# Performance work log

Hardware: AMD Instinct MI355X
Metric: run time of the kernel (lower is better)

## Reference

```python
import jax, jax.numpy as jnp
import numpy as np

L, F = 3, 6                 # levels, temporal abstraction factor
B, T0, E = 64, 36, 1024     # batch, bottom-level timesteps, encoded-obs dim
S, D, H = 128, 1024, 1024   # stoch size, deter (GRU) size, embed size
O = S + D                   # cell 'output' size (posterior sample ++ det_state)
MIN_STD = 1e-4


def _params(key):
    ks = jax.random.split(key, 10)
    w = lambda k, *s: jax.random.normal(k, s, jnp.float32) * 0.02
    z = lambda *s: jnp.zeros(s, jnp.float32)
    return dict(
        w1=w(ks[0], L, S + O, H), b1=z(L, H),
        gru_wi=w(ks[1], L, H, 3 * D), gru_wh=w(ks[2], L, D, 3 * D),
        gru_bi=z(L, 3 * D), gru_bh=z(L, 3 * D),
        w2=w(ks[3], L, D, H), b2=z(L, H),
        wpm=w(ks[4], L, H, S), bpm=z(L, S),
        wps=w(ks[5], L, H, S), bps=z(L, S),
        q1=w(ks[6], L, D + E, H), qb1=z(L, H),
        q2=w(ks[7], L, H, H), qb2=z(L, H),
        wqm=w(ks[8], L, H, S), bqm=z(L, S),
        wqs=w(ks[9], L, H, S), bqs=z(L, S))


def setup_inputs() -> dict:
    key = jax.random.key(0)
    ks = jax.random.split(key, 10)
    inp = {}
    for l in range(L):
        T = T0 // F ** l  # 36, 6, 1
        inp[f"x{l}"] = jax.random.normal(ks[l], (B, T, E), jnp.float32)
        inp[f"np{l}"] = jax.random.normal(ks[3 + l], (B, T, S), jnp.float32)
        inp[f"nq{l}"] = jax.random.normal(ks[6 + l], (B, T, S), jnp.float32)
    inp.update(_params(ks[9]))
    return inp


def _run_level(p, x, context, ep, eq):
    """Scan one RSSM cell over time. x: [B,T,E], context: [B,T,O]."""
    b = x.shape[0]
    init = (jnp.zeros((b, S), x.dtype), jnp.zeros((b, D), x.dtype))

    def step(carry, inp):
        sample, det = carry
        obs, ctx, e_p, e_q = inp
        # --- prior: dense(sample ++ context) -> GRU -> dense -> (mean, std) ---
        h = jax.nn.elu(jnp.concatenate([sample, ctx], -1) @ p["w1"] + p["b1"])
        gi = h @ p["gru_wi"] + p["gru_bi"]
        gh = det @ p["gru_wh"] + p["gru_bh"]
        gi_r, gi_z, gi_n = jnp.split(gi, 3, -1)
        gh_r, gh_z, gh_n = jnp.split(gh, 3, -1)
        r = jax.nn.sigmoid(gi_r + gh_r)
        zt = jax.nn.sigmoid(gi_z + gh_z)
        n = jnp.tanh(gi_n + r * gh_n)
        det_new = (1.0 - zt) * n + zt * det
        h2 = jax.nn.elu(det_new @ p["w2"] + p["b2"])
        p_mean = h2 @ p["wpm"] + p["bpm"]
        p_std = jax.nn.softplus(h2 @ p["wps"] + p["bps"]) + MIN_STD
        p_sample = p_mean + p_std * e_p  # reparameterized prior draw (unused downstream when use_obs)
        # --- posterior: dense(det ++ obs) -> dense -> (mean, std); use_obs=True ---
        hq = jax.nn.elu(jnp.concatenate([det_new, obs], -1) @ p["q1"] + p["qb1"])
        hq = jax.nn.elu(hq @ p["q2"] + p["qb2"])
        q_mean = hq @ p["wqm"] + p["bqm"]
        q_std = jax.nn.softplus(hq @ p["wqs"] + p["bqs"]) + MIN_STD
        q_sample = q_mean + q_std * e_q
        out = jnp.concatenate([q_sample, det_new], -1)  # posterior['output']
        return (q_sample, det_new), out

    xs = tuple(a.swapaxes(0, 1) for a in (x, context, ep, eq))  # time-major
    _, out = jax.lax.scan(step, init, xs)
    return out.swapaxes(0, 1)  # [B, T, O]


def reference(x0, x1, x2, np0, np1, np2, nq0, nq1, nq2,
              w1, b1, gru_wi, gru_wh, gru_bi, gru_bh, w2, b2,
              wpm, bpm, wps, bps, q1, qb1, q2, qb2, wqm, bqm, wqs, bqs):
    params = dict(w1=w1, b1=b1, gru_wi=gru_wi, gru_wh=gru_wh, gru_bi=gru_bi,
                  gru_bh=gru_bh, w2=w2, b2=b2, wpm=wpm, bpm=bpm, wps=wps,
                  bps=bps, q1=q1, qb1=qb1, q2=q2, qb2=qb2, wqm=wqm, bqm=bqm,
                  wqs=wqs, bqs=bqs)
    xs_l, eps, eqs = [x0, x1, x2], [np0, np1, np2], [nq0, nq1, nq2]
    # top level receives zero context of size state_size['output']
    context = jnp.zeros(x2.shape[:2] + (O,), x2.dtype)
    out = None
    for l in range(L - 1, -1, -1):  # top-down, as in CWVAE reversed() loop
        pl = {k: v[l] for k, v in params.items()}
        out = _run_level(pl, xs_l[l], context, eps[l], eqs[l])
        if l > 0:
            # expand_dims+tile+reshape+truncate == repeat along time and crop
            context = jnp.repeat(out, F, axis=1)[:, :xs_l[l - 1].shape[1]]
    return out  # bottom-level posterior 'output': [B, T0, S+D]
```

## Files before the change

### kernel.cpp

```cpp
#include <hip/hip_runtime.h>
#include <hip/hip_bf16.h>
#include <math.h>


#define LVLS 3
#define FACT 6
#define NB 64
#define TT0 36
#define NE 1024
#define NS 128
#define ND 1024
#define NH 1024
#define NO (NS + ND)

typedef __attribute__((ext_vector_type(8))) short bf16x8;
typedef __attribute__((ext_vector_type(4))) float f32x4;
typedef unsigned short u16;

#define MFMA(a, b, c) __builtin_amdgcn_mfma_f32_16x16x32_bf16(a, b, c, 0, 0, 0)

__device__ inline u16 f2bf(float x) {
    unsigned u = __float_as_uint(x);
    unsigned r = u + 0x7fffu + ((u >> 16) & 1u);
    return (u16)(r >> 16);
}

__constant__ const int PFX[10] = {0, 256, 2560, 8704, 14848, 16896, 18944, 20992, 21248, 21504};
__constant__ const int KTS[9]  = {4, 36, 32, 32, 32, 32, 32, 32, 32};

__global__ __launch_bounds__(256) void k_pack_all(
    const float* __restrict__ w1, const float* __restrict__ gwi,
    const float* __restrict__ gwh, const float* __restrict__ q1,
    const float* __restrict__ q2, const float* __restrict__ wqm,
    const float* __restrict__ wqs, u16* __restrict__ dst) {
    int gid = blockIdx.x * 256 + threadIdx.x;
    int fu = gid >> 6, lane = gid & 63;
    int l = fu / 21504, f = fu % 21504;
    int kind = 0;
    while (f >= PFX[kind + 1]) ++kind;
    int local = f - PFX[kind];
    int KT = KTS[kind];
    int kt = local % KT, nt = local / KT;
    int k = kt * 32 + ((lane >> 4) << 3);
    int n = nt * 16 + (lane & 15);
    const float* src;
    int rw;
    switch (kind) {
        case 0: src = w1 + (size_t)l * 1310720 + (size_t)k * 1024 + n; rw = 1024; break;
        case 1: src = w1 + (size_t)l * 1310720 + (size_t)(128 + k) * 1024 + n; rw = 1024; break;
        case 2: src = gwi + (size_t)l * 3145728 + (size_t)k * 3072 + n; rw = 3072; break;
        case 3: src = gwh + (size_t)l * 3145728 + (size_t)k * 3072 + n; rw = 3072; break;
        case 4: src = q1 + (size_t)l * 2097152 + (size_t)k * 1024 + n; rw = 1024; break;
        case 5: src = q1 + (size_t)l * 2097152 + (size_t)(1024 + k) * 1024 + n; rw = 1024; break;
        case 6: src = q2 + (size_t)l * 1048576 + (size_t)k * 1024 + n; rw = 1024; break;
        case 7: src = wqm + (size_t)l * 131072 + (size_t)k * 128 + n; rw = 128; break;
        default: src = wqs + (size_t)l * 131072 + (size_t)k * 128 + n; rw = 128; break;
    }
    bf16x8 v;
#pragma unroll
    for (int e = 0; e < 8; ++e) v[e] = (short)f2bf(src[(size_t)e * rw]);
    reinterpret_cast<bf16x8*>(dst)[(size_t)fu * 64 + lane] = v;
}

__global__ __launch_bounds__(256) void k_gemm_f32(
    const float* __restrict__ A, int ldA, int KT,
    const bf16x8* __restrict__ P, float* __restrict__ out) {
    int lane = threadIdx.x & 63, wave = threadIdx.x >> 6;
    int nt = blockIdx.x;
    int mt = blockIdx.y * 4 + wave;
    f32x4 acc = {};
    const float* a = A + (size_t)(mt * 16 + (lane & 15)) * ldA + ((lane >> 4) << 3);
    for (int kt = 0; kt < KT; ++kt) {
        float4 u0 = *(const float4*)(a + kt * 32);
        float4 u1 = *(const float4*)(a + kt * 32 + 4);
        bf16x8 fv;
        fv[0] = (short)f2bf(u0.x); fv[1] = (short)f2bf(u0.y);
        fv[2] = (short)f2bf(u0.z); fv[3] = (short)f2bf(u0.w);
        fv[4] = (short)f2bf(u1.x); fv[5] = (short)f2bf(u1.y);
        fv[6] = (short)f2bf(u1.z); fv[7] = (short)f2bf(u1.w);
        acc = MFMA(fv, P[((size_t)nt * KT + kt) * 64 + lane], acc);
    }
    int col = nt * 16 + (lane & 15);
    int row0 = mt * 16 + ((lane >> 4) << 2);
#pragma unroll
    for (int j = 0; j < 4; ++j) out[(size_t)(row0 + j) * 1024 + col] = acc[j];
}

template <int KT, bool ELU>
__global__ __launch_bounds__(512) void k_denseX(
    const u16* __restrict__ A, int ldA, const bf16x8* __restrict__ P,
    const float* __restrict__ addp, int addStride, const float* __restrict__ bias,
    u16* __restrict__ outB, int ldO) {
    constexpr int KTH = KT / 2;
    __shared__ f32x4 red[4][64];
    __shared__ u16 ldsT[64][16];
    int tid = threadIdx.x, lane = tid & 63, wave = tid >> 6;
    int m = wave & 3, kh = wave >> 2;
    int nt = blockIdx.x;
    f32x4 acc = {};
    if (A) {
        const u16* a = A + (size_t)(m * 16 + (lane & 15)) * ldA + ((lane >> 4) << 3);
        for (int kt = kh * KTH; kt < kh * KTH + KTH; ++kt) {
            bf16x8 av = *(const bf16x8*)(a + kt * 32);
            acc = MFMA(av, P[((size_t)nt * KT + kt) * 64 + lane], acc);
        }
    }
    if (kh == 1) red[m][lane] = acc;
    __syncthreads();
    if (kh == 0) {
        acc += red[m][lane];
        int col = nt * 16 + (lane & 15);
        float bv = bias[col];
        int row0 = m * 16 + ((lane >> 4) << 2);
#pragma unroll
        for (int j = 0; j < 4; ++j) {
            int row = row0 + j;
            float x = acc[j] + bv;
            if (addp) x += addp[(size_t)row * addStride + col];
            if (ELU) x = x > 0.f ? x : expm1f(x);
            ldsT[row][lane & 15] = f2bf(x);
        }
    }
    __syncthreads();
    if (tid < 128) {
        int row = tid >> 1, seg = tid & 1;
        *(bf16x8*)(outB + (size_t)row * ldO + nt * 16 + seg * 8) =
            *(const bf16x8*)(&ldsT[row][seg * 8]);
    }
}

__global__ __launch_bounds__(512) void k_gru(
    const u16* __restrict__ hA, const u16* __restrict__ dA,
    const float* __restrict__ dF, const bf16x8* __restrict__ Pi,
    const bf16x8* __restrict__ Ph, const float* __restrict__ bi,
    const float* __restrict__ bh, u16* __restrict__ dA_out,
    float* __restrict__ dF_out, float* __restrict__ outp, int outStride) {
    __shared__ f32x4 red[4][6][64];
    __shared__ u16 ldsT[64][16];
    int tid = threadIdx.x, lane = tid & 63, wave = tid >> 6;
    int m = wave & 3, kh = wave >> 2;
    int nt = blockIdx.x;
    f32x4 acc[6] = {};
    const u16* ah = hA + (size_t)(m * 16 + (lane & 15)) * 1024 + ((lane >> 4) << 3);
    const u16* ad = dA ? dA + (size_t)(m * 16 + (lane & 15)) * 1024 + ((lane >> 4) << 3) : nullptr;
    for (int kt = kh * 16; kt < kh * 16 + 16; ++kt) {
        bf16x8 av = *(const bf16x8*)(ah + kt * 32);
#pragma unroll
        for (int g = 0; g < 3; ++g)
            acc[g] = MFMA(av, Pi[((size_t)(g * 64 + nt) * 32 + kt) * 64 + lane], acc[g]);
        if (ad) {
            bf16x8 dv = *(const bf16x8*)(ad + kt * 32);
#pragma unroll
            for (int g = 0; g < 3; ++g)
                acc[3 + g] = MFMA(dv, Ph[((size_t)(g * 64 + nt) * 32 + kt) * 64 + lane], acc[3 + g]);
        }
    }
    if (kh == 1) {
#pragma unroll
        for (int q = 0; q < 6; ++q) red[m][q][lane] = acc[q];
    }
    __syncthreads();
    if (kh == 0) {
#pragma unroll
        for (int q = 0; q < 6; ++q) acc[q] += red[m][q][lane];
        int col = nt * 16 + (lane & 15);
        float bir = bi[col], biz = bi[1024 + col], bin = bi[2048 + col];
        float bhr = bh[col], bhz = bh[1024 + col], bhn = bh[2048 + col];
        int row0 = m * 16 + ((lane >> 4) << 2);
#pragma unroll
        for (int j = 0; j < 4; ++j) {
            int row = row0 + j;
            float r = 1.f / (1.f + expf(-(acc[0][j] + bir + acc[3][j] + bhr)));
            float z = 1.f / (1.f + expf(-(acc[1][j] + biz + acc[4][j] + bhz)));
            float n = tanhf(acc[2][j] + bin + r * (acc[5][j] + bhn));
            float dold = dF ? dF[(size_t)row * 1024 + col] : 0.f;
            float dn = (1.f - z) * n + z * dold;
            dF_out[(size_t)row * 1024 + col] = dn;
            outp[(size_t)row * outStride + 128 + col] = dn;
            ldsT[row][lane & 15] = f2bf(dn);
        }
    }
    __syncthreads();
    if (tid < 128) {
        int row = tid >> 1, seg = tid & 1;
        *(bf16x8*)(dA_out + (size_t)row * 1024 + nt * 16 + seg * 8) =
            *(const bf16x8*)(&ldsT[row][seg * 8]);
    }
}

__global__ __launch_bounds__(512) void k_out(
    const u16* __restrict__ hA, const bf16x8* __restrict__ Pm,
    const bf16x8* __restrict__ Ps, const float* __restrict__ bm,
    const float* __restrict__ bs, const float* __restrict__ nq, int nqStride,
    u16* __restrict__ sampB, float* __restrict__ outp, int outStride) {
    __shared__ f32x4 red[4][2][64];
    __shared__ u16 ldsT[64][16];
    int tid = threadIdx.x, lane = tid & 63, wave = tid >> 6;
    int m = wave & 3, kh = wave >> 2;
    int nt = blockIdx.x;
    f32x4 am = {}, as_ = {};
    const u16* a = hA + (size_t)(m * 16 + (lane & 15)) * 1024 + ((lane >> 4) << 3);
    for (int kt = kh * 16; kt < kh * 16 + 16; ++kt) {
        bf16x8 av = *(const bf16x8*)(a + kt * 32);
        am = MFMA(av, Pm[((size_t)nt * 32 + kt) * 64 + lane], am);
        as_ = MFMA(av, Ps[((size_t)nt * 32 + kt) * 64 + lane], as_);
    }
    if (kh == 1) { red[m][0][lane] = am; red[m][1][lane] = as_; }
    __syncthreads();
    if (kh == 0) {
        am += red[m][0][lane];
        as_ += red[m][1][lane];
        int col = nt * 16 + (lane & 15);
        float bmv = bm[col], bsv = bs[col];
        int row0 = m * 16 + ((lane >> 4) << 2);
#pragma unroll
        for (int j = 0; j < 4; ++j) {
            int row = row0 + j;
            float mean = am[j] + bmv;
            float xs = as_[j] + bsv;
            float sp = fmaxf(xs, 0.f) + log1pf(expf(-fabsf(xs)));
            float q = mean + (sp + 1e-4f) * nq[(size_t)row * nqStride + col];
            outp[(size_t)row * outStride + col] = q;
            ldsT[row][lane & 15] = f2bf(q);
        }
    }
    __syncthreads();
    if (tid < 128) {
        int row = tid >> 1, seg = tid & 1;
        *(bf16x8*)(sampB + (size_t)row * 128 + nt * 16 + seg * 8) =
            *(const bf16x8*)(&ldsT[row][seg * 8]);
    }
}

extern "C" void kernel_launch(void* const* d_in, const int* in_sizes, int n_in,
                              void* d_out, int out_size, void* d_ws, size_t ws_size,
                              hipStream_t stream) {
    (void)n_in; (void)out_size; (void)ws_size;
    int ix[3], inq[3];
    if (in_sizes[1] == NB * TT0 * NS) {
        ix[0] = 0; inq[0] = 2; ix[1] = 3; inq[1] = 5; ix[2] = 6; inq[2] = 8;
    } else {
        ix[0] = 0; ix[1] = 1; ix[2] = 2; inq[0] = 6; inq[1] = 7; inq[2] = 8;
    }
    const float* x[3] = {(const float*)d_in[ix[0]], (const float*)d_in[ix[1]], (const float*)d_in[ix[2]]};
    const float* nqp[3] = {(const float*)d_in[inq[0]], (const float*)d_in[inq[1]], (const float*)d_in[inq[2]]};
    const float* w1w = (const float*)d_in[9];
    const float* b1  = (const float*)d_in[10];
    const float* gwi = (const float*)d_in[11];
    const float* gwh = (const float*)d_in[12];
    const float* gbi = (const float*)d_in[13];
    const float* gbh = (const float*)d_in[14];
    const float* q1w = (const float*)d_in[21];
    const float* qb1 = (const float*)d_in[22];
    const float* q2w = (const float*)d_in[23];
    const float* qb2 = (const float*)d_in[24];
    const float* wqm = (const float*)d_in[25];
    const float* bqm = (const float*)d_in[26];
    const float* wqs = (const float*)d_in[27];
    const float* bqs = (const float*)d_in[28];

    char* wsb = (char*)d_ws;
    size_t off = 0;
    auto alloc = [&](size_t bytes) {
        void* p = wsb + off;
        off = (off + bytes + 255) & ~(size_t)255;
        return p;
    };
    u16* wsW = (u16*)alloc((size_t)64512 * 1024);
    const int Tarr[3] = {36, 6, 1};
    float* obs_pre[3];
    for (int l = 0; l < 3; ++l) obs_pre[l] = (float*)alloc((size_t)NB * Tarr[l] * 1024 * 4);
    float* c_pre[2];
    c_pre[0] = (float*)alloc((size_t)NB * 6 * 1024 * 4);
    c_pre[1] = (float*)alloc((size_t)NB * 1 * 1024 * 4);
    u16* hB   = (u16*)alloc((size_t)NB * 1024 * 2);
    u16* hq1B = (u16*)alloc((size_t)NB * 1024 * 2);
    u16* hq2B = (u16*)alloc((size_t)NB * 1024 * 2);
    u16* detB16[2] = {(u16*)alloc((size_t)NB * 1024 * 2), (u16*)alloc((size_t)NB * 1024 * 2)};
    float* detF[2] = {(float*)alloc((size_t)NB * 1024 * 4), (float*)alloc((size_t)NB * 1024 * 4)};
    u16* sampB = (u16*)alloc((size_t)NB * 128 * 2);
    float* out1 = (float*)alloc((size_t)NB * 6 * NO * 4);
    float* out2 = (float*)alloc((size_t)NB * 1 * NO * 4);

    const int pf[9] = {0, 256, 2560, 8704, 14848, 16896, 18944, 20992, 21248};
    auto Pk = [&](int l, int kind) -> const bf16x8* {
        return (const bf16x8*)wsW + ((size_t)l * 21504 + pf[kind]) * 64;
    };

    k_pack_all<<<16128, 256, 0, stream>>>(w1w, gwi, gwh, q1w, q2w, wqm, wqs, wsW);

    for (int l = 0; l < 3; ++l)
        k_gemm_f32<<<dim3(64, Tarr[l]), 256, 0, stream>>>(x[l], 1024, 32, Pk(l, 5), obs_pre[l]);

    float* outbuf[3] = {(float*)d_out, out1, out2};

    for (int l = 2; l >= 0; --l) {
        int T = Tarr[l];
        if (l < 2) {
            int Tup = Tarr[l + 1];
            k_gemm_f32<<<dim3(64, Tup), 256, 0, stream>>>(outbuf[l + 1], 1152, 36, Pk(l, 1),
                                                          c_pre[l]);
        }
        int Tup = (l == 2) ? 1 : Tarr[l + 1];
        int cur = 1;
        for (int t = 0; t < T; ++t) {
            const u16* sampA = t ? sampB : nullptr;
            const u16* dIn16 = t ? detB16[cur] : nullptr;
            const float* dInF = t ? detF[cur] : nullptr;
            u16* dOut16 = detB16[cur ^ 1];
            float* dOutF = detF[cur ^ 1];
            const float* addw1 = (l == 2) ? nullptr : c_pre[l] + (size_t)(t / FACT) * 1024;
            float* outp = outbuf[l] + (size_t)t * NO;

            k_denseX<4, true><<<64, 512, 0, stream>>>(sampA, 128, Pk(l, 0), addw1, Tup * 1024,
                                                      b1 + l * 1024, hB, 1024);
            k_gru<<<64, 512, 0, stream>>>(hB, dIn16, dInF, Pk(l, 2), Pk(l, 3),
                                          gbi + (size_t)l * 3072, gbh + (size_t)l * 3072, dOut16,
                                          dOutF, outp, T * NO);
            k_denseX<32, true><<<64, 512, 0, stream>>>(dOut16, 1024, Pk(l, 4),
                                                       obs_pre[l] + (size_t)t * 1024, T * 1024,
                                                       qb1 + l * 1024, hq1B, 1024);
            k_denseX<32, true><<<64, 512, 0, stream>>>(hq1B, 1024, Pk(l, 6), nullptr, 0,
                                                       qb2 + l * 1024, hq2B, 1024);
            k_out<<<8, 512, 0, stream>>>(hq2B, Pk(l, 7), Pk(l, 8), bqm + l * 128, bqs + l * 128,
                                         nqp[l] + (size_t)t * 128, T * 128, sampB, outp, T * NO);
            cur ^= 1;
        }
    }
}
```

Measured before the change: 2.478 ms.

## Replace per-step kernel launches with persistent cooperative scan kernel holding weights in LDS

Replaces the five kernel launches per timestep with one cooperative kernel per level. Its 179 blocks each preload their slice of the packed bf16 weights into shared memory once and loop over time, using grid.sync between the dense, GRU-matmul, gate, q1, q2 and output stages. The GRU is split into separate gi/gh matmul blocks that write fp32 pre-activations to global memory, followed by an elementwise gate pass. The fp32-input GEMM is also rewritten to stage A tiles in LDS and compute 64 rows per block. This removes launch overhead and repeated weight reads from global memory, at the cost of six grid-wide barriers per step and extra global traffic for the gi/gh buffers.

```diff
diff --git a/kernel.cpp b/kernel.cpp
--- a/kernel.cpp
+++ b/kernel.cpp
@@ -1,19 +1,19 @@
 #include <hip/hip_runtime.h>
 #include <hip/hip_bf16.h>
+#include <hip/hip_cooperative_groups.h>
 #include <math.h>
 
-
-#define LVLS 3
+namespace cg = cooperative_groups;
+
+
 #define FACT 6
 #define NB 64
 #define TT0 36
-#define NE 1024
-#define NS 128
-#define ND 1024
-#define NH 1024
-#define NO (NS + ND)
+#define GBLK 179
+#define LDS_BYTES 120832
 
 typedef __attribute__((ext_vector_type(8))) short bf16x8;
+typedef __attribute__((ext_vector_type(4))) short bf16x4;
 typedef __attribute__((ext_vector_type(4))) float f32x4;
 typedef unsigned short u16;
 
@@ -62,173 +62,349 @@
     reinterpret_cast<bf16x8*>(dst)[(size_t)fu * 64 + lane] = v;
 }
 
-__global__ __launch_bounds__(256) void k_gemm_f32(
-    const float* __restrict__ A, int ldA, int KT,
+__global__ __launch_bounds__(512) void k_gemm(
+    const float* __restrict__ A, int ldA, int KTtot,
     const bf16x8* __restrict__ P, float* __restrict__ out) {
-    int lane = threadIdx.x & 63, wave = threadIdx.x >> 6;
-    int nt = blockIdx.x;
-    int mt = blockIdx.y * 4 + wave;
-    f32x4 acc = {};
-    const float* a = A + (size_t)(mt * 16 + (lane & 15)) * ldA + ((lane >> 4) << 3);
-    for (int kt = 0; kt < KT; ++kt) {
-        float4 u0 = *(const float4*)(a + kt * 32);
-        float4 u1 = *(const float4*)(a + kt * 32 + 4);
-        bf16x8 fv;
-        fv[0] = (short)f2bf(u0.x); fv[1] = (short)f2bf(u0.y);
-        fv[2] = (short)f2bf(u0.z); fv[3] = (short)f2bf(u0.w);
-        fv[4] = (short)f2bf(u1.x); fv[5] = (short)f2bf(u1.y);
-        fv[6] = (short)f2bf(u1.z); fv[7] = (short)f2bf(u1.w);
-        acc = MFMA(fv, P[((size_t)nt * KT + kt) * 64 + lane], acc);
-    }
-    int col = nt * 16 + (lane & 15);
-    int row0 = mt * 16 + ((lane >> 4) << 2);
-#pragma unroll
-    for (int j = 0; j < 4; ++j) out[(size_t)(row0 + j) * 1024 + col] = acc[j];
+    __shared__ u16 ldsA[64 * 264];
+    int tid = threadIdx.x, lane = tid & 63, wave = tid >> 6;
+    int nt = blockIdx.x * 8 + wave;
+    int y = blockIdx.y;
+    int K = KTtot * 32;
+    int kfo = (lane >> 4) << 3;
+    f32x4 acc[4] = {};
+    for (int k0 = 0; k0 < K; k0 += 256) {
+        int chunk = min(256, K - k0);
+        int cf4 = chunk >> 2;
+        for (int idx = tid; idx < 64 * cf4; idx += 512) {
+            int row = idx / cf4, c4 = idx % cf4;
+            float4 v = *(const float4*)(A + (size_t)(y * 64 + row) * ldA + k0 + c4 * 4);
+            bf16x4 bv;
+            bv[0] = (short)f2bf(v.x); bv[1] = (short)f2bf(v.y);
+            bv[2] = (short)f2bf(v.z); bv[3] = (short)f2bf(v.w);
+            *(bf16x4*)(&ldsA[row * 264 + c4 * 4]) = bv;
+        }
+        __syncthreads();
+        int nkt = chunk >> 5;
+        for (int ktl = 0; ktl < nkt; ++ktl) {
+            int ktg = (k0 >> 5) + ktl;
+#pragma unroll
+            for (int m = 0; m < 4; ++m) {
+                bf16x8 af = *(const bf16x8*)(&ldsA[(m * 16 + (lane & 15)) * 264 + ktl * 32 + kfo]);
+                acc[m] = MFMA(af, P[((size_t)nt * KTtot + ktg) * 64 + lane], acc[m]);
+            }
+        }
+        __syncthreads();
+    }
+    int colL = lane & 15;
+#pragma unroll
+    for (int m = 0; m < 4; ++m) {
+        int row0 = m * 16 + ((lane >> 4) << 2);
+#pragma unroll
+        for (int j = 0; j < 4; ++j)
+            out[(size_t)(y * 64 + row0 + j) * 1024 + nt * 16 + colL] = acc[m][j];
+    }
 }
 
-template <int KT, bool ELU>
-__global__ __launch_bounds__(512) void k_denseX(
-    const u16* __restrict__ A, int ldA, const bf16x8* __restrict__ P,
-    const float* __restrict__ addp, int addStride, const float* __restrict__ bias,
-    u16* __restrict__ outB, int ldO) {
-    constexpr int KTH = KT / 2;
-    __shared__ f32x4 red[4][64];
-    __shared__ u16 ldsT[64][16];
-    int tid = threadIdx.x, lane = tid & 63, wave = tid >> 6;
+struct ScanArgs {
+    const u16* Pw;
+    const float *b1, *gbi, *gbh, *qb1, *qb2, *bqm, *bqs;
+    const float* cpre;
+    const float* obs;
+    const float* nq;
+    float* outp;
+    u16 *hB, *hq1B, *hq2B, *sampB;
+    u16 *det16a, *det16b;
+    float *detFa, *detFb;
+    float *giF, *ghF;
+    int T, Tup;
+};
+
+__global__ void __launch_bounds__(512, 2) k_scan(ScanArgs a) {
+    cg::grid_group grid = cg::this_grid();
+    extern __shared__ char smem[];
+    u16* BIGu = (u16*)smem;
+    u16* HWu = (u16*)(smem + 98304);
+    f32x4* RED = (f32x4*)(smem + 102400);
+    u16* TRp = (u16*)(smem + 114688);
+
+    int b = blockIdx.x, tid = threadIdx.x;
+    int lane = tid & 63, wave = tid >> 6;
     int m = wave & 3, kh = wave >> 2;
-    int nt = blockIdx.x;
-    f32x4 acc = {};
-    if (A) {
-        const u16* a = A + (size_t)(m * 16 + (lane & 15)) * ldA + ((lane >> 4) << 3);
-        for (int kt = kh * KTH; kt < kh * KTH + KTH; ++kt) {
-            bf16x8 av = *(const bf16x8*)(a + kt * 32);
-            acc = MFMA(av, P[((size_t)nt * KT + kt) * 64 + lane], acc);
-        }
-    }
-    if (kh == 1) red[m][lane] = acc;
-    __syncthreads();
-    if (kh == 0) {
-        acc += red[m][lane];
-        int col = nt * 16 + (lane & 15);
-        float bv = bias[col];
-        int row0 = m * 16 + ((lane >> 4) << 2);
-#pragma unroll
-        for (int j = 0; j < 4; ++j) {
-            int row = row0 + j;
-            float x = acc[j] + bv;
-            if (addp) x += addp[(size_t)row * addStride + col];
-            if (ELU) x = x > 0.f ? x : expm1f(x);
-            ldsT[row][lane & 15] = f2bf(x);
-        }
-    }
-    __syncthreads();
-    if (tid < 128) {
-        int row = tid >> 1, seg = tid & 1;
-        *(bf16x8*)(outB + (size_t)row * ldO + nt * 16 + seg * 8) =
-            *(const bf16x8*)(&ldsT[row][seg * 8]);
-    }
-}
-
-__global__ __launch_bounds__(512) void k_gru(
-    const u16* __restrict__ hA, const u16* __restrict__ dA,
-    const float* __restrict__ dF, const bf16x8* __restrict__ Pi,
-    const bf16x8* __restrict__ Ph, const float* __restrict__ bi,
-    const float* __restrict__ bh, u16* __restrict__ dA_out,
-    float* __restrict__ dF_out, float* __restrict__ outp, int outStride) {
-    __shared__ f32x4 red[4][6][64];
-    __shared__ u16 ldsT[64][16];
-    int tid = threadIdx.x, lane = tid & 63, wave = tid >> 6;
-    int m = wave & 3, kh = wave >> 2;
-    int nt = blockIdx.x;
-    f32x4 acc[6] = {};
-    const u16* ah = hA + (size_t)(m * 16 + (lane & 15)) * 1024 + ((lane >> 4) << 3);
-    const u16* ad = dA ? dA + (size_t)(m * 16 + (lane & 15)) * 1024 + ((lane >> 4) << 3) : nullptr;
-    for (int kt = kh * 16; kt < kh * 16 + 16; ++kt) {
-        bf16x8 av = *(const bf16x8*)(ah + kt * 32);
-#pragma unroll
-        for (int g = 0; g < 3; ++g)
-            acc[g] = MFMA(av, Pi[((size_t)(g * 64 + nt) * 32 + kt) * 64 + lane], acc[g]);
-        if (ad) {
-            bf16x8 dv = *(const bf16x8*)(ad + kt * 32);
-#pragma unroll
-            for (int g = 0; g < 3; ++g)
-                acc[3 + g] = MFMA(dv, Ph[((size_t)(g * 64 + nt) * 32 + kt) * 64 + lane], acc[3 + g]);
-        }
-    }
-    if (kh == 1) {
-#pragma unroll
-        for (int q = 0; q < 6; ++q) red[m][q][lane] = acc[q];
-    }
-    __syncthreads();
-    if (kh == 0) {
-#pragma unroll
-        for (int q = 0; q < 6; ++q) acc[q] += red[m][q][lane];
-        int col = nt * 16 + (lane & 15);
-        float bir = bi[col], biz = bi[1024 + col], bin = bi[2048 + col];
-        float bhr = bh[col], bhz = bh[1024 + col], bhn = bh[2048 + col];
-        int row0 = m * 16 + ((lane >> 4) << 2);
-#pragma unroll
-        for (int j = 0; j < 4; ++j) {
-            int row = row0 + j;
-            float r = 1.f / (1.f + expf(-(acc[0][j] + bir + acc[3][j] + bhr)));
-            float z = 1.f / (1.f + expf(-(acc[1][j] + biz + acc[4][j] + bhz)));
-            float n = tanhf(acc[2][j] + bin + r * (acc[5][j] + bhn));
-            float dold = dF ? dF[(size_t)row * 1024 + col] : 0.f;
-            float dn = (1.f - z) * n + z * dold;
-            dF_out[(size_t)row * 1024 + col] = dn;
-            outp[(size_t)row * outStride + 128 + col] = dn;
-            ldsT[row][lane & 15] = f2bf(dn);
-        }
-    }
-    __syncthreads();
-    if (tid < 128) {
-        int row = tid >> 1, seg = tid & 1;
-        *(bf16x8*)(dA_out + (size_t)row * 1024 + nt * 16 + seg * 8) =
-            *(const bf16x8*)(&ldsT[row][seg * 8]);
-    }
-}
-
-__global__ __launch_bounds__(512) void k_out(
-    const u16* __restrict__ hA, const bf16x8* __restrict__ Pm,
-    const bf16x8* __restrict__ Ps, const float* __restrict__ bm,
-    const float* __restrict__ bs, const float* __restrict__ nq, int nqStride,
-    u16* __restrict__ sampB, float* __restrict__ outp, int outStride) {
-    __shared__ f32x4 red[4][2][64];
-    __shared__ u16 ldsT[64][16];
-    int tid = threadIdx.x, lane = tid & 63, wave = tid >> 6;
-    int m = wave & 3, kh = wave >> 2;
-    int nt = blockIdx.x;
-    f32x4 am = {}, as_ = {};
-    const u16* a = hA + (size_t)(m * 16 + (lane & 15)) * 1024 + ((lane >> 4) << 3);
-    for (int kt = kh * 16; kt < kh * 16 + 16; ++kt) {
-        bf16x8 av = *(const bf16x8*)(a + kt * 32);
-        am = MFMA(av, Pm[((size_t)nt * 32 + kt) * 64 + lane], am);
-        as_ = MFMA(av, Ps[((size_t)nt * 32 + kt) * 64 + lane], as_);
-    }
-    if (kh == 1) { red[m][0][lane] = am; red[m][1][lane] = as_; }
-    __syncthreads();
-    if (kh == 0) {
-        am += red[m][0][lane];
-        as_ += red[m][1][lane];
-        int col = nt * 16 + (lane & 15);
-        float bmv = bm[col], bsv = bs[col];
-        int row0 = m * 16 + ((lane >> 4) << 2);
-#pragma unroll
-        for (int j = 0; j < 4; ++j) {
-            int row = row0 + j;
-            float mean = am[j] + bmv;
-            float xs = as_[j] + bsv;
-            float sp = fmaxf(xs, 0.f) + log1pf(expf(-fabsf(xs)));
-            float q = mean + (sp + 1e-4f) * nq[(size_t)row * nqStride + col];
-            outp[(size_t)row * outStride + col] = q;
-            ldsT[row][lane & 15] = f2bf(q);
-        }
-    }
-    __syncthreads();
-    if (tid < 128) {
-        int row = tid >> 1, seg = tid & 1;
-        *(bf16x8*)(sampB + (size_t)row * 128 + nt * 16 + seg * 8) =
-            *(const bf16x8*)(&ldsT[row][seg * 8]);
+    int kfo = (lane >> 4) << 3;
+    int colL = lane & 15;
+    int row0 = m * 16 + ((lane >> 4) << 2);
+    int arow = m * 16 + (lane & 15);
+
+    {
+        const bf16x8* src = (const bf16x8*)a.Pw;
+        bf16x8* dstB = (bf16x8*)BIGu;
+        if (b < 171) {
+#pragma unroll
+            for (int s = 0; s < 3; ++s) {
+                int B = 3 * b + s;
+                if (B < 512) {
+                    long fu;
+                    if (B < 192) fu = 2560 + (long)B * 32;
+                    else if (B < 384) fu = 8704 + (long)(B - 192) * 32;
+                    else if (B < 448) fu = 14848 + (long)(B - 384) * 32;
+                    else fu = 18944 + (long)(B - 448) * 32;
+                    for (int i = 0; i < 4; ++i)
+                        dstB[s * 2048 + tid + i * 512] = src[fu * 64 + tid + i * 512];
+                }
+            }
+            if (b < 64 && tid < 256)
+                ((bf16x8*)HWu)[tid] = src[(long)b * 4 * 64 + tid];
+        } else {
+            int i = b - 171;
+            long fm = 20992 + (long)i * 32, fs = 21248 + (long)i * 32;
+            for (int it = 0; it < 4; ++it) {
+                dstB[tid + it * 512] = src[fm * 64 + tid + it * 512];
+                dstB[2048 + tid + it * 512] = src[fs * 64 + tid + it * 512];
+            }
+        }
+        __syncthreads();
+    }
+
+    auto BIGF = [&](int s, int kt) -> bf16x8 {
+        return *(const bf16x8*)(BIGu + s * 16384 + (kt * 64 + lane) * 8);
+    };
+
+    for (int t = 0; t < a.T; ++t) {
+        int dn = t & 1, dold = dn ^ 1;
+        u16* det16n = dn ? a.det16b : a.det16a;
+        const u16* det16o = dn ? a.det16a : a.det16b;
+        float* detFn = dn ? a.detFb : a.detFa;
+        const float* detFo = dn ? a.detFa : a.detFb;
+
+        if (b < 64) {
+            f32x4 acc = {};
+            if (t > 0) {
+                const u16* ar = a.sampB + (size_t)arow * 128 + kfo;
+                for (int kt = kh * 2; kt < kh * 2 + 2; ++kt) {
+                    bf16x8 av = *(const bf16x8*)(ar + kt * 32);
+                    acc = MFMA(av, *(const bf16x8*)(HWu + (kt * 64 + lane) * 8), acc);
+                }
+            }
+            if (kh) RED[m * 64 + lane] = acc;
+            __syncthreads();
+            if (!kh) {
+                acc += RED[m * 64 + lane];
+                int col = b * 16 + colL;
+                float bv = a.b1[col];
+#pragma unroll
+                for (int j = 0; j < 4; ++j) {
+                    int row = row0 + j;
+                    float x = acc[j] + bv;
+                    if (a.cpre)
+                        x += a.cpre[(size_t)(t / FACT) * 1024 + (size_t)row * a.Tup * 1024 + col];
+                    x = x > 0.f ? x : expm1f(x);
+                    TRp[row * 16 + colL] = f2bf(x);
+                }
+            }
+            __syncthreads();
+            if (tid < 128) {
+                int row = tid >> 1, seg = tid & 1;
+                *(bf16x8*)(a.hB + (size_t)row * 1024 + b * 16 + seg * 8) =
+                    *(const bf16x8*)(TRp + row * 16 + seg * 8);
+            }
+        }
+        grid.sync();
+
+        if (b < 128) {
+            bool isgh = b >= 64;
+            f32x4 acc[3] = {};
+            if (!isgh || t > 0) {
+                const u16* Ab = isgh ? det16o : a.hB;
+                const u16* ar = Ab + (size_t)arow * 1024 + kfo;
+                for (int kt = kh * 16; kt < kh * 16 + 16; ++kt) {
+                    bf16x8 av = *(const bf16x8*)(ar + kt * 32);
+                    acc[0] = MFMA(av, BIGF(0, kt), acc[0]);
+                    acc[1] = MFMA(av, BIGF(1, kt), acc[1]);
+                    acc[2] = MFMA(av, BIGF(2, kt), acc[2]);
+                }
+            }
+            if (kh) {
+#pragma unroll
+                for (int s = 0; s < 3; ++s) RED[(s * 4 + m) * 64 + lane] = acc[s];
+            }
+            __syncthreads();
+            if (!kh) {
+                float* O = isgh ? a.ghF : a.giF;
+                int base = b * 3 - (isgh ? 192 : 0);
+#pragma unroll
+                for (int s = 0; s < 3; ++s) {
+                    f32x4 v = acc[s] + RED[(s * 4 + m) * 64 + lane];
+                    int c = (base + s) * 16 + colL;
+#pragma unroll
+                    for (int j = 0; j < 4; ++j) O[(size_t)(row0 + j) * 3072 + c] = v[j];
+                }
+            }
+        }
+        grid.sync();
+
+        {
+            int i = b * 512 + tid;
+            if (i < 65536) {
+                int row = i >> 10, col = i & 1023;
+                size_t o = (size_t)row * 3072 + col;
+                float gir = a.giF[o], giz = a.giF[o + 1024], gin = a.giF[o + 2048];
+                float ghr = a.ghF[o], ghz = a.ghF[o + 1024], ghn = a.ghF[o + 2048];
+                float r = 1.f / (1.f + expf(-(gir + a.gbi[col] + ghr + a.gbh[col])));
+                float z = 1.f / (1.f + expf(-(giz + a.gbi[1024 + col] + ghz + a.gbh[1024 + col])));
+                float n = tanhf(gin + a.gbi[2048 + col] + r * (ghn + a.gbh[2048 + col]));
+                float dov = t ? detFo[i] : 0.f;
+                float dnv = (1.f - z) * n + z * dov;
+                detFn[i] = dnv;
+                det16n[i] = f2bf(dnv);
+                a.outp[(size_t)row * a.T * 1152 + (size_t)t * 1152 + 128 + col] = dnv;
+            }
+        }
+        grid.sync();
+
+        {
+            unsigned mask = 0;
+#pragma unroll
+            for (int s = 0; s < 3; ++s) {
+                int B = 3 * b + s;
+                if (B >= 384 && B < 448) mask |= 1u << s;
+            }
+            if (mask) {
+                f32x4 acc[3] = {};
+                const u16* ar = det16n + (size_t)arow * 1024 + kfo;
+                for (int kt = kh * 16; kt < kh * 16 + 16; ++kt) {
+                    bf16x8 av = *(const bf16x8*)(ar + kt * 32);
+                    if (mask & 1u) acc[0] = MFMA(av, BIGF(0, kt), acc[0]);
+                    if (mask & 2u) acc[1] = MFMA(av, BIGF(1, kt), acc[1]);
+                    if (mask & 4u) acc[2] = MFMA(av, BIGF(2, kt), acc[2]);
+                }
+                if (kh) {
+#pragma unroll
+                    for (int s = 0; s < 3; ++s)
+                        if ((mask >> s) & 1u) RED[(s * 4 + m) * 64 + lane] = acc[s];
+                }
+                __syncthreads();
+                if (!kh) {
+#pragma unroll
+                    for (int s = 0; s < 3; ++s)
+                        if ((mask >> s) & 1u) {
+                            f32x4 v = acc[s] + RED[(s * 4 + m) * 64 + lane];
+                            int cb = 3 * b + s - 384;
+                            int col = cb * 16 + colL;
+#pragma unroll
+                            for (int j = 0; j < 4; ++j) {
+                                int row = row0 + j;
+                                float x = v[j] + a.qb1[col] +
+                                          a.obs[(size_t)t * 1024 + (size_t)row * a.T * 1024 + col];
+                                x = x > 0.f ? x : expm1f(x);
+                                TRp[s * 1024 + row * 16 + colL] = f2bf(x);
+                            }
+                        }
+                }
+                __syncthreads();
+                if (tid < 384) {
+                    int s = tid >> 7;
+                    if ((mask >> s) & 1u) {
+                        int r2 = tid & 127, row = r2 >> 1, seg = r2 & 1;
+                        int cb = 3 * b + s - 384;
+                        *(bf16x8*)(a.hq1B + (size_t)row * 1024 + cb * 16 + seg * 8) =
+                            *(const bf16x8*)(TRp + s * 1024 + row * 16 + seg * 8);
+                    }
+                }
+            }
+        }
+        grid.sync();
+
+        {
+            unsigned mask = 0;
+#pragma unroll
+            for (int s = 0; s < 3; ++s) {
+                int B = 3 * b + s;
+                if (B >= 448 && B < 512) mask |= 1u << s;
+            }
+            if (mask) {
+                f32x4 acc[3] = {};
+                const u16* ar = a.hq1B + (size_t)arow * 1024 + kfo;
+                for (int kt = kh * 16; kt < kh * 16 + 16; ++kt) {
+                    bf16x8 av = *(const bf16x8*)(ar + kt * 32);
+                    if (mask & 1u) acc[0] = MFMA(av, BIGF(0, kt), acc[0]);
+                    if (mask & 2u) acc[1] = MFMA(av, BIGF(1, kt), acc[1]);
+                    if (mask & 4u) acc[2] = MFMA(av, BIGF(2, kt), acc[2]);
+                }
+                if (kh) {
+#pragma unroll
+                    for (int s = 0; s < 3; ++s)
+                        if ((mask >> s) & 1u) RED[(s * 4 + m) * 64 + lane] = acc[s];
+                }
+                __syncthreads();
+                if (!kh) {
+#pragma unroll
+                    for (int s = 0; s < 3; ++s)
+                        if ((mask >> s) & 1u) {
+                            f32x4 v = acc[s] + RED[(s * 4 + m) * 64 + lane];
+                            int cb = 3 * b + s - 448;
+                            int col = cb * 16 + colL;
+#pragma unroll
+                            for (int j = 0; j < 4; ++j) {
+                                int row = row0 + j;
+                                float x = v[j] + a.qb2[col];
+                                x = x > 0.f ? x : expm1f(x);
+                                TRp[s * 1024 + row * 16 + colL] = f2bf(x);
+                            }
+                        }
+                }
+                __syncthreads();
+                if (tid < 384) {
+                    int s = tid >> 7;
+                    if ((mask >> s) & 1u) {
+                        int r2 = tid & 127, row = r2 >> 1, seg = r2 & 1;
+                        int cb = 3 * b + s - 448;
+                        *(bf16x8*)(a.hq2B + (size_t)row * 1024 + cb * 16 + seg * 8) =
+                            *(const bf16x8*)(TRp + s * 1024 + row * 16 + seg * 8);
+                    }
+                }
+            }
+        }
+        grid.sync();
+
+        if (b >= 171) {
+            int i = b - 171;
+            f32x4 am = {}, as_ = {};
+            const u16* ar = a.hq2B + (size_t)arow * 1024 + kfo;
+            for (int kt = kh * 16; kt < kh * 16 + 16; ++kt) {
+                bf16x8 av = *(const bf16x8*)(ar + kt * 32);
+                am = MFMA(av, BIGF(0, kt), am);
+                as_ = MFMA(av, BIGF(1, kt), as_);
+            }
+            if (kh) {
+                RED[(0 * 4 + m) * 64 + lane] = am;
+                RED[(1 * 4 + m) * 64 + lane] = as_;
+            }
+            __syncthreads();
+            if (!kh) {
+                am += RED[(0 * 4 + m) * 64 + lane];
+                as_ += RED[(1 * 4 + m) * 64 + lane];
+                int col = i * 16 + colL;
+                float bmv = a.bqm[col], bsv = a.bqs[col];
+#pragma unroll
+                for (int j = 0; j < 4; ++j) {
+                    int row = row0 + j;
+                    float mean = am[j] + bmv;
+                    float xs = as_[j] + bsv;
+                    float sp = fmaxf(xs, 0.f) + log1pf(expf(-fabsf(xs)));
+                    float q = mean + (sp + 1e-4f) *
+                                         a.nq[(size_t)t * 128 + (size_t)row * a.T * 128 + col];
+                    a.outp[(size_t)row * a.T * 1152 + (size_t)t * 1152 + col] = q;
+                    TRp[row * 16 + colL] = f2bf(q);
+                }
+            }
+            __syncthreads();
+            if (tid < 128) {
+                int row = tid >> 1, seg = tid & 1;
+                *(bf16x8*)(a.sampB + (size_t)row * 128 + i * 16 + seg * 8) =
+                    *(const bf16x8*)(TRp + row * 16 + seg * 8);
+            }
+        }
+        grid.sync();
     }
 }
 
@@ -237,7 +413,7 @@
                               hipStream_t stream) {
     (void)n_in; (void)out_size; (void)ws_size;
     int ix[3], inq[3];
-    if (in_sizes[1] == NB * TT0 * NS) {
+    if (in_sizes[1] == NB * TT0 * 128) {
         ix[0] = 0; inq[0] = 2; ix[1] = 3; inq[1] = 5; ix[2] = 6; inq[2] = 8;
     } else {
         ix[0] = 0; ix[1] = 1; ix[2] = 2; inq[0] = 6; inq[1] = 7; inq[2] = 8;
@@ -276,11 +452,15 @@
     u16* hB   = (u16*)alloc((size_t)NB * 1024 * 2);
     u16* hq1B = (u16*)alloc((size_t)NB * 1024 * 2);
     u16* hq2B = (u16*)alloc((size_t)NB * 1024 * 2);
-    u16* detB16[2] = {(u16*)alloc((size_t)NB * 1024 * 2), (u16*)alloc((size_t)NB * 1024 * 2)};
-    float* detF[2] = {(float*)alloc((size_t)NB * 1024 * 4), (float*)alloc((size_t)NB * 1024 * 4)};
+    u16* det16a = (u16*)alloc((size_t)NB * 1024 * 2);
+    u16* det16b = (u16*)alloc((size_t)NB * 1024 * 2);
+    float* detFa = (float*)alloc((size_t)NB * 1024 * 4);
+    float* detFb = (float*)alloc((size_t)NB * 1024 * 4);
+    float* giF = (float*)alloc((size_t)NB * 3072 * 4);
+    float* ghF = (float*)alloc((size_t)NB * 3072 * 4);
     u16* sampB = (u16*)alloc((size_t)NB * 128 * 2);
-    float* out1 = (float*)alloc((size_t)NB * 6 * NO * 4);
-    float* out2 = (float*)alloc((size_t)NB * 1 * NO * 4);
+    float* out1 = (float*)alloc((size_t)NB * 6 * 1152 * 4);
+    float* out2 = (float*)alloc((size_t)NB * 1 * 1152 * 4);
 
     const int pf[9] = {0, 256, 2560, 8704, 14848, 16896, 18944, 20992, 21248};
     auto Pk = [&](int l, int kind) -> const bf16x8* {
@@ -290,41 +470,34 @@
     k_pack_all<<<16128, 256, 0, stream>>>(w1w, gwi, gwh, q1w, q2w, wqm, wqs, wsW);
 
     for (int l = 0; l < 3; ++l)
-        k_gemm_f32<<<dim3(64, Tarr[l]), 256, 0, stream>>>(x[l], 1024, 32, Pk(l, 5), obs_pre[l]);
+        k_gemm<<<dim3(8, Tarr[l]), 512, 0, stream>>>(x[l], 1024, 32, Pk(l, 5), obs_pre[l]);
 
     float* outbuf[3] = {(float*)d_out, out1, out2};
 
     for (int l = 2; l >= 0; --l) {
-        int T = Tarr[l];
-        if (l < 2) {
-            int Tup = Tarr[l + 1];
-            k_gemm_f32<<<dim3(64, Tup), 256, 0, stream>>>(outbuf[l + 1], 1152, 36, Pk(l, 1),
-                                                          c_pre[l]);
-        }
         int Tup = (l == 2) ? 1 : Tarr[l + 1];
-        int cur = 1;
-        for (int t = 0; t < T; ++t) {
-            const u16* sampA = t ? sampB : nullptr;
-            const u16* dIn16 = t ? detB16[cur] : nullptr;
-            const float* dInF = t ? detF[cur] : nullptr;
-            u16* dOut16 = detB16[cur ^ 1];
-            float* dOutF = detF[cur ^ 1];
-            const float* addw1 = (l == 2) ? nullptr : c_pre[l] + (size_t)(t / FACT) * 1024;
-            float* outp = outbuf[l] + (size_t)t * NO;
-
-            k_denseX<4, true><<<64, 512, 0, stream>>>(sampA, 128, Pk(l, 0), addw1, Tup * 1024,
-                                                      b1 + l * 1024, hB, 1024);
-            k_gru<<<64, 512, 0, stream>>>(hB, dIn16, dInF, Pk(l, 2), Pk(l, 3),
-                                          gbi + (size_t)l * 3072, gbh + (size_t)l * 3072, dOut16,
-                                          dOutF, outp, T * NO);
-            k_denseX<32, true><<<64, 512, 0, stream>>>(dOut16, 1024, Pk(l, 4),
-                                                       obs_pre[l] + (size_t)t * 1024, T * 1024,
-                                                       qb1 + l * 1024, hq1B, 1024);
-            k_denseX<32, true><<<64, 512, 0, stream>>>(hq1B, 1024, Pk(l, 6), nullptr, 0,
-                                                       qb2 + l * 1024, hq2B, 1024);
-            k_out<<<8, 512, 0, stream>>>(hq2B, Pk(l, 7), Pk(l, 8), bqm + l * 128, bqs + l * 128,
-                                         nqp[l] + (size_t)t * 128, T * 128, sampB, outp, T * NO);
-            cur ^= 1;
-        }
+        if (l < 2)
+            k_gemm<<<dim3(8, Tup), 512, 0, stream>>>(outbuf[l + 1], 1152, 36, Pk(l, 1), c_pre[l]);
+
+        ScanArgs sa;
+        sa.Pw = wsW + (size_t)l * 21504 * 512;
+        sa.b1 = b1 + (size_t)l * 1024;
+        sa.gbi = gbi + (size_t)l * 3072;
+        sa.gbh = gbh + (size_t)l * 3072;
+        sa.qb1 = qb1 + (size_t)l * 1024;
+        sa.qb2 = qb2 + (size_t)l * 1024;
+        sa.bqm = bqm + (size_t)l * 128;
+        sa.bqs = bqs + (size_t)l * 128;
+        sa.cpre = (l == 2) ? nullptr : c_pre[l];
+        sa.obs = obs_pre[l];
+        sa.nq = nqp[l];
+        sa.outp = outbuf[l];
+        sa.hB = hB; sa.hq1B = hq1B; sa.hq2B = hq2B; sa.sampB = sampB;
+        sa.det16a = det16a; sa.det16b = det16b;
+        sa.detFa = detFa; sa.detFb = detFb;
+        sa.giF = giF; sa.ghF = ghF;
+        sa.T = Tarr[l]; sa.Tup = Tup;
+        void* kp[] = {&sa};
+        hipLaunchCooperativeKernel((void*)k_scan, dim3(GBLK), dim3(512), kp, LDS_BYTES, stream);
     }
 }
```

Result: slower. 7.150 ms (+188.6%).
